# Kernel optimization log

Hardware: AMD Instinct MI355X
Metric: run time of the kernel (lower is better)

Reference implementation:

```python
import jax, jax.numpy as jnp
import numpy as np

B, N, INDIM = 512, 200, 200
D1, D2, D3 = 32, 32, 8
RATIO = 0.5
K1 = int(np.ceil(RATIO * N))    # 100 nodes kept after pool1
K2 = int(np.ceil(RATIO * K1))   # 50 nodes kept after pool2
BN_EPS = 1e-5
NEG = -1e9


def setup_inputs() -> dict:
    key = jax.random.key(0)
    ks = jax.random.split(key, 16)
    x = jax.random.normal(ks[0], (B, N, INDIM), jnp.float32)
    u = jax.random.uniform(ks[1], (B, N, N), jnp.float32)
    ut = jnp.triu(jnp.where(u > 0.9, u, 0.0), 1)
    adj = ut + jnp.swapaxes(ut, 1, 2)
    g = lambda i, shape: jax.random.normal(ks[i], shape, jnp.float32) * 0.1
    return dict(
        x=x, adj=adj,
        W1=g(2, (INDIM, D1)), a1s=g(3, (D1,)), a1d=g(4, (D1,)), b1=jnp.zeros((D1,), jnp.float32),
        W2=g(5, (D1, D2)), a2s=g(6, (D2,)), a2d=g(7, (D2,)), b2=jnp.zeros((D2,), jnp.float32),
        pw1=g(8, (D1,)), pw2=g(9, (D2,)),
        fc1_w=g(10, ((D1 + D2) * 2, D2)), fc1_b=jnp.zeros((D2,), jnp.float32),
        fc2_w=g(11, (D2, D3)), fc2_b=jnp.zeros((D3,), jnp.float32),
        fc3_w=g(12, (D3, 2)), fc3_b=jnp.zeros((2,), jnp.float32),
        bn4_g=jnp.ones((D2,), jnp.float32), bn4_b=jnp.zeros((D2,), jnp.float32),
        bn5_g=jnp.ones((D3,), jnp.float32), bn5_b=jnp.zeros((D3,), jnp.float32))


def _gat(x, mask, W, a_s, a_d, b):
    # PyG GATConv (heads=1): alpha_ij = softmax_j LeakyReLU(a_d.h_i + a_s.h_j) over in-neighbors j (self-loops added)
    h = jnp.einsum('bnf,fd->bnd', x, W)
    es = h @ a_s                    # [B,n] source term
    ed = h @ a_d                    # [B,n] dest term
    m = mask | jnp.eye(mask.shape[1], dtype=bool)
    logits = jax.nn.leaky_relu(ed[:, :, None] + es[:, None, :], 0.2)
    alpha = jax.nn.softmax(jnp.where(m, logits, NEG), axis=-1)   # [B,n,n]
    return jnp.einsum('bij,bjd->bid', alpha, h) + b


def _topk(x, adj_w, w, k):
    # TopKPooling(multiplier=1, nonlinearity=sigmoid): score = sigmoid(x.w/||w||)
    score = jax.nn.sigmoid((x @ w) / (jnp.linalg.norm(w) + 1e-16))   # [B,n]
    vals, idx = jax.lax.top_k(score, k)                              # perm sorted desc, as PyG
    xk = jnp.take_along_axis(x, idx[:, :, None], axis=1) * vals[:, :, None]
    ak = jnp.take_along_axis(jnp.take_along_axis(adj_w, idx[:, :, None], axis=1), idx[:, None, :], axis=2)
    return xk, ak, vals


def _bn(z, g, b):
    # eval-mode BatchNorm1d: running_mean=0, running_var=1
    return g * z / jnp.sqrt(1.0 + BN_EPS) + b


def reference(x, adj, W1, a1s, a1d, b1, W2, a2s, a2d, b2, pw1, pw2,
              fc1_w, fc1_b, fc2_w, fc2_b, fc3_w, fc3_b, bn4_g, bn4_b, bn5_g, bn5_b):
    h = _gat(x, adj > 0, W1, a1s, a1d, b1)
    h, aw, s1 = _topk(h, adj, pw1, K1)
    x1 = jnp.concatenate([h.max(axis=1), h.mean(axis=1)], axis=1)    # [B, 64]
    # augment_adj: add self-loops, spspmm (A+I)@(A+I), remove self-loops
    eye = jnp.eye(K1, dtype=aw.dtype)
    a2 = jnp.einsum('bij,bjk->bik', aw + eye, aw + eye) * (1.0 - eye)
    h = _gat(h, a2 != 0, W2, a2s, a2d, b2)
    h, _, s2 = _topk(h, a2, pw2, K2)
    x2 = jnp.concatenate([h.max(axis=1), h.mean(axis=1)], axis=1)    # [B, 64]
    z = jnp.concatenate([x1, x2], axis=1)                            # [B, 128]
    z = _bn(jax.nn.relu(z @ fc1_w + fc1_b), bn4_g, bn4_b)            # dropout: eval -> identity
    z = _bn(jax.nn.relu(z @ fc2_w + fc2_b), bn5_g, bn5_b)
    logp = jax.nn.log_softmax(z @ fc3_w + fc3_b, axis=-1)            # [B, 2]
    return logp, s1, s2
```

## Files before the change

kernel.cpp:

```cpp
#include <hip/hip_runtime.h>
#include <math.h>

#define N_   200
#define B_   512
#define K1_  100
#define K2_  50

#define S1_OFF 1024
#define S2_OFF 52224

__device__ __forceinline__ float lrelu(float v) { return v > 0.f ? v : 0.2f * v; }
__device__ __forceinline__ float sigm(float v)  { return 1.f / (1.f + __expf(-v)); }

__device__ __forceinline__ void bitonic_desc(float* key, int* idx, int n, int t) {
  for (int k = 2; k <= n; k <<= 1) {
    for (int j = k >> 1; j > 0; j >>= 1) {
      __syncthreads();
      int ixj = t ^ j;
      if (t < n && ixj > t) {
        float a = key[t], c = key[ixj];
        int ia = idx[t], ic = idx[ixj];
        bool gt = (a > c) || (a == c && ia < ic);
        if (((t & k) == 0) ? !gt : gt) {
          key[t] = c; key[ixj] = a; idx[t] = ic; idx[ixj] = ia;
        }
      }
    }
  }
  __syncthreads();
}


__global__ __launch_bounds__(256) void gnn_fused(
    const float* __restrict__ x, const float* __restrict__ adj,
    const float* __restrict__ W1, const float* __restrict__ a1s,
    const float* __restrict__ a1d, const float* __restrict__ b1,
    const float* __restrict__ W2g, const float* __restrict__ a2s,
    const float* __restrict__ a2d, const float* __restrict__ b2,
    const float* __restrict__ pw1, const float* __restrict__ pw2,
    const float* __restrict__ fc1w, const float* __restrict__ fc1b,
    const float* __restrict__ fc2w, const float* __restrict__ fc2b,
    const float* __restrict__ fc3w, const float* __restrict__ fc3b,
    const float* __restrict__ bn4g, const float* __restrict__ bn4b,
    const float* __restrict__ bn5g, const float* __restrict__ bn5b,
    float* __restrict__ out)
{
  __shared__ __align__(16) char smem[38192];
  float*    sH    = (float*)smem;
  float*    sXK   = sH + 100 * 32;
  float*    sES   = (float*)(smem + 25600);
  float*    sED   = (float*)(smem + 26400);
  unsigned* sBITS = (unsigned*)(smem + 27200);
  float*    sW2   = (float*)(smem + 27200);
  float*    sKey  = (float*)(smem + 32800);
  int*      sIdx  = (int*)(smem + 33824);
  int*      sSel  = (int*)(smem + 34848);
  float*    sVal  = (float*)(smem + 35248);
  float*    sXV   = (float*)(smem + 35648);
  float*    sRed  = (float*)(smem + 36160);
  unsigned* sMask2= (unsigned*)(smem + 36192);

  const int t = threadIdx.x;
  const int b = blockIdx.x;
  const float* xb = x   + (size_t)b * N_ * N_;
  const float* ab = adj + (size_t)b * N_ * N_;

  if (t < N_) {
    float acc[32];
    #pragma unroll
    for (int d = 0; d < 32; ++d) acc[d] = 0.f;
    const float* xr = xb + t * N_;
    for (int k = 0; k < N_; k += 4) {
      float4 xv = *(const float4*)(xr + k);
      #pragma unroll
      for (int kk = 0; kk < 4; ++kk) {
        float xs = (&xv.x)[kk];
        const float* wr = W1 + (k + kk) * 32;
        #pragma unroll
        for (int d = 0; d < 32; ++d) acc[d] += xs * wr[d];
      }
    }
    float es = 0.f, ed = 0.f;
    #pragma unroll
    for (int d = 0; d < 32; ++d) { es += acc[d] * a1s[d]; ed += acc[d] * a1d[d]; }
    sES[t] = es; sED[t] = ed;
    #pragma unroll
    for (int d = 0; d < 32; ++d) sH[t * 32 + d] = acc[d];
  }
  __syncthreads();

  {
    float v = (t < N_) ? sES[t] : -3.0e38f;
    #pragma unroll
    for (int off = 1; off < 64; off <<= 1) v = fmaxf(v, __shfl_xor(v, off, 64));
    if ((t & 63) == 0) sRed[t >> 6] = v;
  }
  __syncthreads();
  {
    float esmax = fmaxf(fmaxf(sRed[0], sRed[1]), fmaxf(sRed[2], sRed[3]));

    float acc[32];
    if (t < N_) {
      const float* arow = ab + (size_t)t * N_;
      float ed_i = sED[t];
      float L = lrelu(ed_i + esmax);
      float ssum = 0.f;
      #pragma unroll
      for (int d = 0; d < 32; ++d) acc[d] = 0.f;
      for (int jw = 0; jw < 7; ++jw) {
        int jbase = jw * 32;
        int cnt = (jw < 6) ? 32 : 8;
        unsigned mb = 0u;
        for (int j4 = 0; j4 < cnt; j4 += 4) {
          float4 av = *(const float4*)(arow + jbase + j4);
          #pragma unroll
          for (int jj = 0; jj < 4; ++jj) {
            int j = jbase + j4 + jj;
            float a = (&av.x)[jj];
            bool conn = a > 0.f;
            if (conn) mb |= (1u << (j4 + jj));
            float w = 0.f;
            if (conn || j == t) w = __expf(lrelu(ed_i + sES[j]) - L);
            ssum += w;
            const float* hr = &sH[j * 32];
            #pragma unroll
            for (int d = 0; d < 32; ++d) acc[d] += w * hr[d];
          }
        }
        sBITS[t * 7 + jw] = mb;
      }
      float inv = 1.f / ssum;
      #pragma unroll
      for (int d = 0; d < 32; ++d) acc[d] = acc[d] * inv + b1[d];
    }
    __syncthreads();
    if (t < N_) {
      #pragma unroll
      for (int d = 0; d < 32; ++d) sH[t * 32 + d] = acc[d];
    }
  }
  __syncthreads();

  {
    float npw = 0.f;
    #pragma unroll
    for (int d = 0; d < 32; ++d) npw += pw1[d] * pw1[d];
    npw = sqrtf(npw) + 1e-16f;
    float sc = -1.f;
    if (t < N_) {
      float dp = 0.f;
      #pragma unroll
      for (int d = 0; d < 32; ++d) dp += sH[t * 32 + d] * pw1[d];
      sc = sigm(dp / npw);
    }
    sKey[t] = sc; sIdx[t] = t;
  }
  bitonic_desc(sKey, sIdx, 256, t);
  if (t < K1_) {
    out[S1_OFF + b * K1_ + t] = sKey[t];
    sVal[t] = sKey[t]; sSel[t] = sIdx[t];
  }
  __syncthreads();
  {
    float tmp[13];
    #pragma unroll
    for (int it = 0; it < 13; ++it) {
      int i = t + it * 256;
      if (i < K1_ * 32) tmp[it] = sH[sSel[i >> 5] * 32 + (i & 31)] * sVal[i >> 5];
    }
    __syncthreads();
    #pragma unroll
    for (int it = 0; it < 13; ++it) {
      int i = t + it * 256;
      if (i < K1_ * 32) sXK[i] = tmp[it];
    }
  }
  __syncthreads();
  if (t < 32) {
    float m = -3.0e38f, s = 0.f;
    for (int r = 0; r < K1_; ++r) { float v = sXK[r * 32 + t]; m = fmaxf(m, v); s += v; }
    sXV[t] = m; sXV[32 + t] = s / 100.f;
  }

  if (t < K1_) {
    int gi = sSel[t];
    #pragma unroll
    for (int w = 0; w < 4; ++w) {
      unsigned m = 0;
      const int lim = (w < 3) ? 32 : 4;
      for (int jj = 0; jj < lim; ++jj) {
        int j = w * 32 + jj;
        int gj = sSel[j];
        unsigned bit = (sBITS[gi * 7 + (gj >> 5)] >> (gj & 31)) & 1u;
        if (j == t) bit = 1u;
        m |= bit << jj;
      }
      sMask2[t * 5 + w] = m;
    }
  }
  __syncthreads();
  for (int i = t; i < 1024; i += 256) sW2[i] = W2g[i];
  {
    unsigned pr0 = 0, pr1 = 0, pr2 = 0, pr3 = 0;
    if (t < K1_) {
      #pragma unroll
      for (int kw = 0; kw < 4; ++kw) {
        unsigned mk = sMask2[t * 5 + kw];
        const int lim = (kw < 3) ? 32 : 4;
        for (int kk = 0; kk < lim; ++kk) {
          if ((mk >> kk) & 1u) {
            int k = kw * 32 + kk;
            pr0 |= sMask2[k * 5 + 0]; pr1 |= sMask2[k * 5 + 1];
            pr2 |= sMask2[k * 5 + 2]; pr3 |= sMask2[k * 5 + 3];
          }
        }
      }
    }
    __syncthreads();
    if (t < K1_) {
      sMask2[t * 5 + 0] = pr0; sMask2[t * 5 + 1] = pr1;
      sMask2[t * 5 + 2] = pr2; sMask2[t * 5 + 3] = pr3;
    }
  }
  __syncthreads();

  if (t < K1_) {
    float xk[32];
    #pragma unroll
    for (int k = 0; k < 32; ++k) xk[k] = sXK[t * 32 + k];
    float acc[32];
    #pragma unroll
    for (int d = 0; d < 32; ++d) acc[d] = 0.f;
    #pragma unroll
    for (int k = 0; k < 32; ++k) {
      float xv = xk[k];
      const float* wr = &sW2[k * 32];
      #pragma unroll
      for (int d = 0; d < 32; ++d) acc[d] += xv * wr[d];
    }
    float es = 0.f, ed = 0.f;
    #pragma unroll
    for (int d = 0; d < 32; ++d) { es += acc[d] * a2s[d]; ed += acc[d] * a2d[d]; }
    sES[t] = es; sED[t] = ed;
    #pragma unroll
    for (int d = 0; d < 32; ++d) sH[t * 32 + d] = acc[d];
  }
  __syncthreads();
  {
    float v = (t < K1_) ? sES[t] : -3.0e38f;
    #pragma unroll
    for (int off = 1; off < 64; off <<= 1) v = fmaxf(v, __shfl_xor(v, off, 64));
    if ((t & 63) == 0) sRed[t >> 6] = v;
  }
  __syncthreads();
  {
    float esm2 = fmaxf(fmaxf(sRed[0], sRed[1]), fmaxf(sRed[2], sRed[3]));
    float acc[32];
    if (t < K1_) {
      float ed_i = sED[t];
      float L = lrelu(ed_i + esm2);
      float ssum = 0.f;
      #pragma unroll
      for (int d = 0; d < 32; ++d) acc[d] = 0.f;
      #pragma unroll
      for (int jw = 0; jw < 4; ++jw) {
        unsigned mw = sMask2[t * 5 + jw];
        const int lim = (jw < 3) ? 32 : 4;
        for (int jj = 0; jj < lim; ++jj) {
          int j = jw * 32 + jj;
          float w = 0.f;
          if ((mw >> jj) & 1u) w = __expf(lrelu(ed_i + sES[j]) - L);
          ssum += w;
          const float* hr = &sH[j * 32];
          #pragma unroll
          for (int d = 0; d < 32; ++d) acc[d] += w * hr[d];
        }
      }
      float inv = 1.f / ssum;
      #pragma unroll
      for (int d = 0; d < 32; ++d) acc[d] = acc[d] * inv + b2[d];
    }
    __syncthreads();
    if (t < K1_) {
      #pragma unroll
      for (int d = 0; d < 32; ++d) sH[t * 32 + d] = acc[d];
    }
  }
  __syncthreads();

  {
    float npw = 0.f;
    #pragma unroll
    for (int d = 0; d < 32; ++d) npw += pw2[d] * pw2[d];
    npw = sqrtf(npw) + 1e-16f;
    float sc = -1.f;
    if (t < K1_) {
      float dp = 0.f;
      #pragma unroll
      for (int d = 0; d < 32; ++d) dp += sH[t * 32 + d] * pw2[d];
      sc = sigm(dp / npw);
    }
    if (t < 128) { sKey[t] = sc; sIdx[t] = t; }
  }
  bitonic_desc(sKey, sIdx, 128, t);
  if (t < K2_) {
    out[S2_OFF + b * K2_ + t] = sKey[t];
    sVal[t] = sKey[t]; sSel[t] = sIdx[t];
  }
  __syncthreads();
  {
    int d = t & 31, r0 = t >> 5;
    for (int r = r0; r < K2_; r += 8) sXK[r * 32 + d] = sH[sSel[r] * 32 + d] * sVal[r];
  }
  __syncthreads();
  if (t < 32) {
    float m = -3.0e38f, s = 0.f;
    for (int r = 0; r < K2_; ++r) { float v = sXK[r * 32 + t]; m = fmaxf(m, v); s += v; }
    sXV[64 + t] = m; sXV[96 + t] = s / 50.f;
  }
  __syncthreads();

  const float RS = 0.99999500003749969f;
  if (t < 32) {
    float z = fc1b[t];
    for (int k = 0; k < 128; ++k) z += sXV[k] * fc1w[k * 32 + t];
    z = fmaxf(z, 0.f);
    z = bn4g[t] * z * RS + bn4b[t];
    sKey[t] = z;
  }
  __syncthreads();
  if (t < 8) {
    float z = fc2b[t];
    for (int k = 0; k < 32; ++k) z += sKey[k] * fc2w[k * 8 + t];
    z = fmaxf(z, 0.f);
    z = bn5g[t] * z * RS + bn5b[t];
    sKey[32 + t] = z;
  }
  __syncthreads();
  if (t < 2) {
    float z = fc3b[t];
    for (int k = 0; k < 8; ++k) z += sKey[32 + k] * fc3w[k * 2 + t];
    sKey[40 + t] = z;
  }
  __syncthreads();
  if (t < 2) {
    float z0 = sKey[40], z1 = sKey[41];
    float m = fmaxf(z0, z1);
    float lse = m + logf(__expf(z0 - m) + __expf(z1 - m));
    out[b * 2 + t] = sKey[40 + t] - lse;
  }
}

extern "C" void kernel_launch(void* const* d_in, const int* in_sizes, int n_in,
                              void* d_out, int out_size, void* d_ws, size_t ws_size,
                              hipStream_t stream) {
  (void)in_sizes; (void)n_in; (void)d_ws; (void)ws_size; (void)out_size;
  const float* x    = (const float*)d_in[0];
  const float* adj  = (const float*)d_in[1];
  const float* W1   = (const float*)d_in[2];
  const float* a1s  = (const float*)d_in[3];
  const float* a1d  = (const float*)d_in[4];
  const float* b1   = (const float*)d_in[5];
  const float* W2   = (const float*)d_in[6];
  const float* a2s  = (const float*)d_in[7];
  const float* a2d  = (const float*)d_in[8];
  const float* b2   = (const float*)d_in[9];
  const float* pw1  = (const float*)d_in[10];
  const float* pw2  = (const float*)d_in[11];
  const float* fc1w = (const float*)d_in[12];
  const float* fc1b = (const float*)d_in[13];
  const float* fc2w = (const float*)d_in[14];
  const float* fc2b = (const float*)d_in[15];
  const float* fc3w = (const float*)d_in[16];
  const float* fc3b = (const float*)d_in[17];
  const float* bn4g = (const float*)d_in[18];
  const float* bn4b = (const float*)d_in[19];
  const float* bn5g = (const float*)d_in[20];
  const float* bn5b = (const float*)d_in[21];

  gnn_fused<<<B_, 256, 0, stream>>>(x, adj, W1, a1s, a1d, b1, W2, a2s, a2d, b2,
                                    pw1, pw2, fc1w, fc1b, fc2w, fc2b, fc3w, fc3b,
                                    bn4g, bn4b, bn5g, bn5b, (float*)d_out);
}
```

Baseline: 333.8 us.

## Use compacted neighbor lists for GAT1, padded smem rows, rank-based top-k

GAT layer 1 now first builds a per-node byte list of neighbors (plus self) in shared memory, then aggregates only over those, instead of doing a 32-wide FMA for every one of the 200 columns. This removes most of the dense work, since the adjacency is about 10% dense. Shared-memory rows are padded to a stride of 36 so the row reads can use float4 loads with fewer bank conflicts. The bitonic sorts are replaced by a counting rank selection that needs far fewer barriers. Shared memory grows to about 66KB, which may reduce the number of blocks resident per CU, and the list capacity of 128 assumes no node has more neighbors than that.

Measured after the change: 339.9 us. No clear change (+1.8%).

```diff
diff --git a/kernel.cpp b/kernel.cpp
--- a/kernel.cpp
+++ b/kernel.cpp
@@ -1,34 +1,18 @@
 #include <hip/hip_runtime.h>
 #include <math.h>
 
-#define N_   200
-#define B_   512
-#define K1_  100
-#define K2_  50
+#define N_    200
+#define B_    512
+#define K1_   100
+#define K2_   50
+#define ST    36
+#define NBCAP 128
 
 #define S1_OFF 1024
 #define S2_OFF 52224
 
 __device__ __forceinline__ float lrelu(float v) { return v > 0.f ? v : 0.2f * v; }
 __device__ __forceinline__ float sigm(float v)  { return 1.f / (1.f + __expf(-v)); }
-
-__device__ __forceinline__ void bitonic_desc(float* key, int* idx, int n, int t) {
-  for (int k = 2; k <= n; k <<= 1) {
-    for (int j = k >> 1; j > 0; j >>= 1) {
-      __syncthreads();
-      int ixj = t ^ j;
-      if (t < n && ixj > t) {
-        float a = key[t], c = key[ixj];
-        int ia = idx[t], ic = idx[ixj];
-        bool gt = (a > c) || (a == c && ia < ic);
-        if (((t & k) == 0) ? !gt : gt) {
-          key[t] = c; key[ixj] = a; idx[t] = ic; idx[ixj] = ia;
-        }
-      }
-    }
-  }
-  __syncthreads();
-}
 
 
 __global__ __launch_bounds__(256) void gnn_fused(
@@ -45,20 +29,20 @@
     const float* __restrict__ bn5g, const float* __restrict__ bn5b,
     float* __restrict__ out)
 {
-  __shared__ __align__(16) char smem[38192];
-  float*    sH    = (float*)smem;
-  float*    sXK   = sH + 100 * 32;
-  float*    sES   = (float*)(smem + 25600);
-  float*    sED   = (float*)(smem + 26400);
-  unsigned* sBITS = (unsigned*)(smem + 27200);
-  float*    sW2   = (float*)(smem + 27200);
-  float*    sKey  = (float*)(smem + 32800);
-  int*      sIdx  = (int*)(smem + 33824);
-  int*      sSel  = (int*)(smem + 34848);
-  float*    sVal  = (float*)(smem + 35248);
-  float*    sXV   = (float*)(smem + 35648);
-  float*    sRed  = (float*)(smem + 36160);
-  unsigned* sMask2= (unsigned*)(smem + 36192);
+  __shared__ __align__(16) char smem[65968];
+  float*         sH    = (float*)smem;
+  float*         sXK   = sH + 100 * ST;
+  unsigned*      sBITS = (unsigned*)(smem + 28800);
+  float*         sW2   = (float*)(smem + 28800);
+  unsigned char* sNbr  = (unsigned char*)(smem + 34400);
+  float*         sES   = (float*)(smem + 60000);
+  float*         sED   = (float*)(smem + 60800);
+  float*         sKey  = (float*)(smem + 61600);
+  int*           sSel  = (int*)(smem + 62624);
+  float*         sVal  = (float*)(smem + 63024);
+  float*         sXV   = (float*)(smem + 63424);
+  float*         sRed  = (float*)(smem + 63936);
+  unsigned*      sMask2= (unsigned*)(smem + 63968);
 
   const int t = threadIdx.x;
   const int b = blockIdx.x;
@@ -85,7 +69,7 @@
     for (int d = 0; d < 32; ++d) { es += acc[d] * a1s[d]; ed += acc[d] * a1d[d]; }
     sES[t] = es; sED[t] = ed;
     #pragma unroll
-    for (int d = 0; d < 32; ++d) sH[t * 32 + d] = acc[d];
+    for (int d = 0; d < 32; ++d) sH[t * ST + d] = acc[d];
   }
   __syncthreads();
 
@@ -102,33 +86,43 @@
     float acc[32];
     if (t < N_) {
       const float* arow = ab + (size_t)t * N_;
-      float ed_i = sED[t];
-      float L = lrelu(ed_i + esmax);
-      float ssum = 0.f;
-      #pragma unroll
-      for (int d = 0; d < 32; ++d) acc[d] = 0.f;
+      unsigned char* nl = sNbr + t * NBCAP;
+      int cnt = 0;
       for (int jw = 0; jw < 7; ++jw) {
         int jbase = jw * 32;
-        int cnt = (jw < 6) ? 32 : 8;
+        int lim = (jw < 6) ? 32 : 8;
         unsigned mb = 0u;
-        for (int j4 = 0; j4 < cnt; j4 += 4) {
+        for (int j4 = 0; j4 < lim; j4 += 4) {
           float4 av = *(const float4*)(arow + jbase + j4);
           #pragma unroll
           for (int jj = 0; jj < 4; ++jj) {
             int j = jbase + j4 + jj;
-            float a = (&av.x)[jj];
-            bool conn = a > 0.f;
-            if (conn) mb |= (1u << (j4 + jj));
-            float w = 0.f;
-            if (conn || j == t) w = __expf(lrelu(ed_i + sES[j]) - L);
-            ssum += w;
-            const float* hr = &sH[j * 32];
-            #pragma unroll
-            for (int d = 0; d < 32; ++d) acc[d] += w * hr[d];
+            bool conn = (&av.x)[jj] > 0.f;
+            if (conn) mb |= 1u << (j4 + jj);
+            if (conn || j == t) nl[cnt++] = (unsigned char)j;
           }
         }
         sBITS[t * 7 + jw] = mb;
       }
+      float ed_i = sED[t];
+      float L = lrelu(ed_i + esmax);
+      float ssum = 0.f;
+      #pragma unroll
+      for (int d = 0; d < 32; ++d) acc[d] = 0.f;
+      for (int i = 0; i < cnt; ++i) {
+        int j = nl[i];
+        float w = __expf(lrelu(ed_i + sES[j]) - L);
+        ssum += w;
+        const float* hr = &sH[j * ST];
+        #pragma unroll
+        for (int c = 0; c < 8; ++c) {
+          float4 hv = *(const float4*)(hr + c * 4);
+          acc[c * 4 + 0] += w * hv.x;
+          acc[c * 4 + 1] += w * hv.y;
+          acc[c * 4 + 2] += w * hv.z;
+          acc[c * 4 + 3] += w * hv.w;
+        }
+      }
       float inv = 1.f / ssum;
       #pragma unroll
       for (int d = 0; d < 32; ++d) acc[d] = acc[d] * inv + b1[d];
@@ -136,7 +130,7 @@
     __syncthreads();
     if (t < N_) {
       #pragma unroll
-      for (int d = 0; d < 32; ++d) sH[t * 32 + d] = acc[d];
+      for (int d = 0; d < 32; ++d) sH[t * ST + d] = acc[d];
     }
   }
   __syncthreads();
@@ -150,15 +144,26 @@
     if (t < N_) {
       float dp = 0.f;
       #pragma unroll
-      for (int d = 0; d < 32; ++d) dp += sH[t * 32 + d] * pw1[d];
+      for (int d = 0; d < 32; ++d) dp += sH[t * ST + d] * pw1[d];
       sc = sigm(dp / npw);
     }
-    sKey[t] = sc; sIdx[t] = t;
-  }
-  bitonic_desc(sKey, sIdx, 256, t);
-  if (t < K1_) {
-    out[S1_OFF + b * K1_ + t] = sKey[t];
-    sVal[t] = sKey[t]; sSel[t] = sIdx[t];
+    sKey[t] = sc;
+  }
+  __syncthreads();
+  if (t < N_) {
+    float sc = sKey[t];
+    int rank = 0;
+    for (int j = 0; j < N_; j += 4) {
+      #pragma unroll
+      for (int jj = 0; jj < 4; ++jj) {
+        float o = sKey[j + jj];
+        rank += (o > sc || (o == sc && (j + jj) < t)) ? 1 : 0;
+      }
+    }
+    if (rank < K1_) {
+      sSel[rank] = t; sVal[rank] = sc;
+      out[S1_OFF + b * K1_ + rank] = sc;
+    }
   }
   __syncthreads();
   {
@@ -166,19 +171,19 @@
     #pragma unroll
     for (int it = 0; it < 13; ++it) {
       int i = t + it * 256;
-      if (i < K1_ * 32) tmp[it] = sH[sSel[i >> 5] * 32 + (i & 31)] * sVal[i >> 5];
+      if (i < K1_ * 32) tmp[it] = sH[sSel[i >> 5] * ST + (i & 31)] * sVal[i >> 5];
     }
     __syncthreads();
     #pragma unroll
     for (int it = 0; it < 13; ++it) {
       int i = t + it * 256;
-      if (i < K1_ * 32) sXK[i] = tmp[it];
+      if (i < K1_ * 32) sXK[(i >> 5) * ST + (i & 31)] = tmp[it];
     }
   }
   __syncthreads();
   if (t < 32) {
     float m = -3.0e38f, s = 0.f;
-    for (int r = 0; r < K1_; ++r) { float v = sXK[r * 32 + t]; m = fmaxf(m, v); s += v; }
+    for (int r = 0; r < K1_; ++r) { float v = sXK[r * ST + t]; m = fmaxf(m, v); s += v; }
     sXV[t] = m; sXV[32 + t] = s / 100.f;
   }
 
@@ -227,7 +232,7 @@
   if (t < K1_) {
     float xk[32];
     #pragma unroll
-    for (int k = 0; k < 32; ++k) xk[k] = sXK[t * 32 + k];
+    for (int c = 0; c < 8; ++c) *(float4*)&xk[c * 4] = *(const float4*)&sXK[t * ST + c * 4];
     float acc[32];
     #pragma unroll
     for (int d = 0; d < 32; ++d) acc[d] = 0.f;
@@ -243,7 +248,7 @@
     for (int d = 0; d < 32; ++d) { es += acc[d] * a2s[d]; ed += acc[d] * a2d[d]; }
     sES[t] = es; sED[t] = ed;
     #pragma unroll
-    for (int d = 0; d < 32; ++d) sH[t * 32 + d] = acc[d];
+    for (int d = 0; d < 32; ++d) sH[t * ST + d] = acc[d];
   }
   __syncthreads();
   {
@@ -271,7 +276,7 @@
           float w = 0.f;
           if ((mw >> jj) & 1u) w = __expf(lrelu(ed_i + sES[j]) - L);
           ssum += w;
-          const float* hr = &sH[j * 32];
+          const float* hr = &sH[j * ST];
           #pragma unroll
           for (int d = 0; d < 32; ++d) acc[d] += w * hr[d];
         }
@@ -283,7 +288,7 @@
     __syncthreads();
     if (t < K1_) {
       #pragma unroll
-      for (int d = 0; d < 32; ++d) sH[t * 32 + d] = acc[d];
+      for (int d = 0; d < 32; ++d) sH[t * ST + d] = acc[d];
     }
   }
   __syncthreads();
@@ -293,29 +298,38 @@
     #pragma unroll
     for (int d = 0; d < 32; ++d) npw += pw2[d] * pw2[d];
     npw = sqrtf(npw) + 1e-16f;
-    float sc = -1.f;
     if (t < K1_) {
       float dp = 0.f;
       #pragma unroll
-      for (int d = 0; d < 32; ++d) dp += sH[t * 32 + d] * pw2[d];
-      sc = sigm(dp / npw);
-    }
-    if (t < 128) { sKey[t] = sc; sIdx[t] = t; }
-  }
-  bitonic_desc(sKey, sIdx, 128, t);
-  if (t < K2_) {
-    out[S2_OFF + b * K2_ + t] = sKey[t];
-    sVal[t] = sKey[t]; sSel[t] = sIdx[t];
+      for (int d = 0; d < 32; ++d) dp += sH[t * ST + d] * pw2[d];
+      sKey[t] = sigm(dp / npw);
+    }
+  }
+  __syncthreads();
+  if (t < K1_) {
+    float sc = sKey[t];
+    int rank = 0;
+    for (int j = 0; j < K1_; j += 4) {
+      #pragma unroll
+      for (int jj = 0; jj < 4; ++jj) {
+        float o = sKey[j + jj];
+        rank += (o > sc || (o == sc && (j + jj) < t)) ? 1 : 0;
+      }
+    }
+    if (rank < K2_) {
+      sSel[rank] = t; sVal[rank] = sc;
+      out[S2_OFF + b * K2_ + rank] = sc;
+    }
   }
   __syncthreads();
   {
     int d = t & 31, r0 = t >> 5;
-    for (int r = r0; r < K2_; r += 8) sXK[r * 32 + d] = sH[sSel[r] * 32 + d] * sVal[r];
+    for (int r = r0; r < K2_; r += 8) sXK[r * ST + d] = sH[sSel[r] * ST + d] * sVal[r];
   }
   __syncthreads();
   if (t < 32) {
     float m = -3.0e38f, s = 0.f;
-    for (int r = 0; r < K2_; ++r) { float v = sXK[r * 32 + t]; m = fmaxf(m, v); s += v; }
+    for (int r = 0; r < K2_; ++r) { float v = sXK[r * ST + t]; m = fmaxf(m, v); s += v; }
     sXV[64 + t] = m; sXV[96 + t] = s / 50.f;
   }
   __syncthreads();
```
